# Kernel tuning notes

Measured on AMD Instinct MI355X. Metric: run time of the kernel, lower is better.

Reference implementation:

```python
import jax, jax.numpy as jnp
import numpy as np
from jax import lax

B, N, G, K, D = 16, 8192, 512, 32, 128
MLP = [128, 128, 256]
EPS = 1e-5


def setup_inputs() -> dict:
    key = jax.random.key(0)
    ks = jax.random.split(key, 2 + len(MLP))
    inp = {
        "xyz": jax.random.normal(ks[0], (B, N, 3), jnp.float32),
        "points": jax.random.normal(ks[1], (B, N, D), jnp.float32),
    }
    last = D
    for li, oc in enumerate(MLP, 1):
        inp[f"W{li}"] = jax.random.normal(ks[1 + li], (oc, last), jnp.float32) / np.float32(np.sqrt(last))
        inp[f"b{li}"] = jnp.zeros((oc,), jnp.float32)
        inp[f"g{li}"] = jnp.ones((oc,), jnp.float32)
        inp[f"be{li}"] = jnp.zeros((oc,), jnp.float32)
        last = oc
    return inp


def _fps(xyz, num_group):
    # farthest point sampling, deterministic start at index 0 -> idx [B, G]
    b, n, _ = xyz.shape
    init_idx = jnp.zeros((b,), jnp.int32)

    def step(carry, _):
        dists, last_idx = carry                                   # [B,N], [B]
        last = jnp.take_along_axis(xyz, last_idx[:, None, None], axis=1)  # [B,1,3]
        d = jnp.sum((xyz - last) ** 2, axis=-1)                   # [B,N]
        dists = jnp.minimum(dists, d)
        nxt = jnp.argmax(dists, axis=1).astype(jnp.int32)
        return (dists, nxt), nxt

    init = (jnp.full((b, n), 1e10, jnp.float32), init_idx)
    _, rest = lax.scan(step, init, None, length=num_group - 1)    # [G-1, B]
    return jnp.concatenate([init_idx[None, :], rest], axis=0).T   # [B, G]


def _forward(xyz, points, layers):
    b = xyz.shape[0]
    center_idx = _fps(xyz, G)                                       # [B,G]
    center = jnp.take_along_axis(xyz, center_idx[:, :, None], axis=1)  # [B,G,3]
    # KNN: pairwise squared distances center->points, top-k smallest
    d2 = (jnp.sum(center ** 2, -1)[:, :, None]
          + jnp.sum(xyz ** 2, -1)[:, None, :]
          - 2.0 * jnp.einsum("bgc,bnc->bgn", center, xyz))          # [B,G,N]
    _, idx = lax.top_k(-d2, K)                                      # [B,G,K]
    feats = jnp.take_along_axis(points, idx.reshape(b, G * K, 1), axis=1)
    feats = feats.reshape(b, G, K, -1)                              # [B,G,K,D]
    x = feats.transpose(0, 3, 2, 1)                                 # [B,D,K,G]
    for (W, bb, g, be) in layers:
        x = jnp.einsum("oc,bckg->bokg", W, x) + bb[None, :, None, None]
        m = jnp.mean(x, axis=(0, 2, 3), keepdims=True)
        v = jnp.var(x, axis=(0, 2, 3), keepdims=True)               # biased, as torch BN
        x = (x - m) * lax.rsqrt(v + EPS) * g[None, :, None, None] + be[None, :, None, None]
        x = jax.nn.relu(x)
    new_points = jnp.max(x, axis=2).transpose(0, 2, 1)              # [B,G,C_out]
    return center, new_points


def reference(xyz, points, W1, b1, g1, be1, W2, b2, g2, be2, W3, b3, g3, be3):
    layers = [(W1, b1, g1, be1), (W2, b2, g2, be2), (W3, b3, g3, be3)]
    return _forward(xyz, points, layers)
```

## Files before the change

kernel.cpp:

```cpp
#include <hip/hip_runtime.h>
#include <hip/hip_bf16.h>

#define BB 16
#define NN 8192
#define GG 512
#define KK 32
#define DD 128

typedef __attribute__((ext_vector_type(8))) short bf16x8;
typedef __attribute__((ext_vector_type(4))) float f32x4;
typedef __attribute__((ext_vector_type(2))) float f32x2;
typedef __attribute__((ext_vector_type(2))) unsigned int u32x2;
typedef __attribute__((ext_vector_type(4))) unsigned int u32x4;
typedef __attribute__((ext_vector_type(2))) unsigned long long u64x2;

__device__ __forceinline__ unsigned short f2bf(float f){
  unsigned int u = __builtin_bit_cast(unsigned int, f);
  unsigned int r = (u + 0x7FFFu + ((u >> 16) & 1u)) >> 16;
  return (unsigned short)r;
}
__device__ __forceinline__ float bf2f(unsigned short h){
  unsigned int u = ((unsigned int)h) << 16;
  return __builtin_bit_cast(float, u);
}

__device__ __forceinline__ float wave_max_f32(float v){
  int x = __builtin_bit_cast(int, v);
#define STEPMAX(C) { int y = __builtin_amdgcn_update_dpp(x, x, C, 0xF, 0xF, false); \
  float f = fmaxf(__builtin_bit_cast(float,x), __builtin_bit_cast(float,y)); x = __builtin_bit_cast(int,f); }
  STEPMAX(0x111) STEPMAX(0x112) STEPMAX(0x114) STEPMAX(0x118) STEPMAX(0x142) STEPMAX(0x143)
#undef STEPMAX
  return __builtin_bit_cast(float, __builtin_amdgcn_readlane(x, 63));
}
__device__ __forceinline__ float wave_min_f32(float v){
  int x = __builtin_bit_cast(int, v);
#define STEPMIN(C) { int y = __builtin_amdgcn_update_dpp(x, x, C, 0xF, 0xF, false); \
  float f = fminf(__builtin_bit_cast(float,x), __builtin_bit_cast(float,y)); x = __builtin_bit_cast(int,f); }
  STEPMIN(0x111) STEPMIN(0x112) STEPMIN(0x114) STEPMIN(0x118) STEPMIN(0x142) STEPMIN(0x143)
#undef STEPMIN
  return __builtin_bit_cast(float, __builtin_amdgcn_readlane(x, 63));
}
__device__ __forceinline__ int wave_min_i32(int v){
  int x = v;
#define STEPMNI(C) { int y = __builtin_amdgcn_update_dpp(x, x, C, 0xF, 0xF, false); \
  x = (y < x) ? y : x; }
  STEPMNI(0x111) STEPMNI(0x112) STEPMNI(0x114) STEPMNI(0x118) STEPMNI(0x142) STEPMNI(0x143)
#undef STEPMNI
  return __builtin_amdgcn_readlane(x, 63);
}

__device__ __forceinline__ void knn_group(int bg, int t128,
    const float* __restrict__ xs, const float* __restrict__ ys,
    const float* __restrict__ zs, const float* __restrict__ pps,
    const float* __restrict__ center, int* __restrict__ kidx,
    unsigned long long (*wlist)[KK], int* outidx)
{
#pragma clang fp contract(off)
  int lane = t128 & 63, w = t128 >> 6;
  int b = bg >> 9;
  const float cx = center[(size_t)bg*3+0];
  const float cy = center[(size_t)bg*3+1];
  const float cz = center[(size_t)bg*3+2];
  const float ccv = (cx*cx + cy*cy) + cz*cz;
  const float* xb = xs  + (size_t)b*NN;
  const float* yb = ys  + (size_t)b*NN;
  const float* zb = zs  + (size_t)b*NN;
  const float* pb = pps + (size_t)b*NN;

  f32x2 d2v[32];
  float gmin[8]; int gidx[8];
#pragma unroll
  for (int gi = 0; gi < 8; ++gi){ gmin[gi] = 3.4e38f; gidx[gi] = 0x7FFFFFFF; }
  int nb = w*128 + 2*lane;
  f32x2 cxv = (f32x2){cx, cx}, cyv = (f32x2){cy, cy}, czv = (f32x2){cz, cz};
  f32x2 ccvv = (f32x2){ccv, ccv};
#pragma unroll
  for (int q = 0; q < 32; ++q){
    int n0 = q*256 + nb;
    f32x2 x = *(const f32x2*)(xb + n0);
    f32x2 y = *(const f32x2*)(yb + n0);
    f32x2 z = *(const f32x2*)(zb + n0);
    f32x2 pp = *(const f32x2*)(pb + n0);
    f32x2 dot = (cxv*x + cyv*y) + czv*z;
    f32x2 d = (ccvv + pp) - 2.0f*dot;
    d2v[q] = d;
    int gi = q >> 2;
    if (d.x < gmin[gi]){ gmin[gi] = d.x; gidx[gi] = n0; }
    if (d.y < gmin[gi]){ gmin[gi] = d.y; gidx[gi] = n0 + 1; }
  }
  float bv = gmin[0]; int bi = gidx[0];
#pragma unroll
  for (int gi = 1; gi < 8; ++gi)
    if (gmin[gi] < bv){ bv = gmin[gi]; bi = gidx[gi]; }

  unsigned long long mykey = ~0ULL;
  for (int k = 0; k < KK; ++k){
    float wmin = wave_min_f32(bv);
    unsigned long long mask = __ballot(bv == wmin);
    int n_win;
    if (__popcll(mask) == 1){
      n_win = __builtin_amdgcn_readlane(bi, (int)__builtin_ctzll(mask));
    } else {
      int cand = (bv == wmin) ? bi : 0x7FFFFFFF;
      n_win = wave_min_i32(cand);
    }
    if (lane == k){
      unsigned int fm = __builtin_bit_cast(unsigned int, wmin);
      unsigned int mapd = fm ^ (unsigned int)(((int)fm >> 31) | 0x80000000);
      mykey = ((unsigned long long)mapd << 32) | (unsigned int)n_win;
    }
    if (bi == n_win){
#define RESCAN2(GI) { \
      float nm = 3.4e38f; int ni = 0x7FFFFFFF; \
      _Pragma("unroll") \
      for (int j = 0; j < 4; ++j){ \
        int q = GI*4 + j; \
        int n0 = q*256 + nb; \
        f32x2 v = d2v[q]; \
        if (n0 == n_win) v.x = 3.4e38f; \
        if (n0 + 1 == n_win) v.y = 3.4e38f; \
        d2v[q] = v; \
        if (v.x < nm){ nm = v.x; ni = n0; } \
        if (v.y < nm){ nm = v.y; ni = n0 + 1; } } \
      gmin[GI] = nm; gidx[GI] = ni; }
      switch (n_win >> 10){
        case 0: RESCAN2(0); break;
        case 1: RESCAN2(1); break;
        case 2: RESCAN2(2); break;
        case 3: RESCAN2(3); break;
        case 4: RESCAN2(4); break;
        case 5: RESCAN2(5); break;
        case 6: RESCAN2(6); break;
        default: RESCAN2(7); break;
      }
#undef RESCAN2
      bv = gmin[0]; bi = gidx[0];
#pragma unroll
      for (int gi = 1; gi < 8; ++gi)
        if (gmin[gi] < bv){ bv = gmin[gi]; bi = gidx[gi]; }
    }
  }

  if (lane < KK) wlist[w][lane] = mykey;
  __syncthreads();
  if (lane < KK){
    unsigned long long K = mykey;
    const unsigned long long* other = wlist[1 - w];
    int cnt = 0;
#pragma unroll
    for (int j = 0; j < KK; ++j) cnt += (other[j] < K) ? 1 : 0;
    int rank = lane + cnt;
    if (rank < KK) outidx[rank] = (int)(unsigned int)K;
  }
  __syncthreads();
  if (t128 < KK) kidx[(size_t)bg*KK + t128] = outidx[t128];
}

__global__ __launch_bounds__(1024)
void fps_a_kernel(const float* __restrict__ xyz, const float* __restrict__ points,
                  const float* __restrict__ W1, const float* __restrict__ W2,
                  const float* __restrict__ W3,
                  float* __restrict__ center_out, float* __restrict__ ddws,
                  float* __restrict__ xs, float* __restrict__ ys,
                  float* __restrict__ zs, float* __restrict__ pps,
                  unsigned short* __restrict__ Wbf,
                  unsigned short* __restrict__ pointsbf)
{
#pragma clang fp contract(off)
  __shared__ unsigned long long slot[3][2] __attribute__((aligned(16)));
  __shared__ float tbl[NN][4] __attribute__((aligned(16)));
  __shared__ float outbuf[GG][4] __attribute__((aligned(16)));
  int t = threadIdx.x;
  if (blockIdx.x >= BB){
    int pb = blockIdx.x - BB;
    size_t i = ((size_t)pb*1024 + t)*8;
    f32x4 u0 = *(const f32x4*)(points + i);
    f32x4 u1 = *(const f32x4*)(points + i + 4);
    unsigned int w0 = f2bf(u0[0]) | ((unsigned int)f2bf(u0[1]) << 16);
    unsigned int w1 = f2bf(u0[2]) | ((unsigned int)f2bf(u0[3]) << 16);
    unsigned int w2 = f2bf(u1[0]) | ((unsigned int)f2bf(u1[1]) << 16);
    unsigned int w3 = f2bf(u1[2]) | ((unsigned int)f2bf(u1[3]) << 16);
    u32x4 pv = {w0, w1, w2, w3};
    *(u32x4*)(pointsbf + i) = pv;
    if (pb < 128){
      int n = pb*1024 + t;
      float x = xyz[(size_t)n*3 + 0];
      float y = xyz[(size_t)n*3 + 1];
      float z = xyz[(size_t)n*3 + 2];
      xs[n] = x; ys[n] = y; zs[n] = z;
      pps[n] = (x*x + y*y) + z*z;
    }
    if (pb < 64){
      int n = pb*1024 + t;
      float v;
      if (n < 16384)      v = W1[n];
      else if (n < 32768) v = W2[n - 16384];
      else                v = W3[n - 32768];
      Wbf[n] = f2bf(v);
    }
    return;
  }
  int b = blockIdx.x;
  int lane = t & 63, wid = t >> 6;
  const float* base = xyz + (size_t)b * NN * 3;
  f32x2 px[4], py[4], pz[4], dd[4];
#pragma unroll
  for (int i = 0; i < 4; ++i){
    int n0 = i*2048 + t, n1 = n0 + 1024;
    float x0 = base[n0*3+0], y0 = base[n0*3+1], z0 = base[n0*3+2];
    float x1 = base[n1*3+0], y1 = base[n1*3+1], z1 = base[n1*3+2];
    px[i] = (f32x2){x0, x1}; py[i] = (f32x2){y0, y1}; pz[i] = (f32x2){z0, z1};
    dd[i] = (f32x2){1e10f, 1e10f};
    f32x4 c0 = {x0, y0, z0, 0.f}, c1 = {x1, y1, z1, 0.f};
    *(f32x4*)&tbl[n0][0] = c0;
    *(f32x4*)&tbl[n1][0] = c1;
  }
  float lx = base[0], ly = base[1], lz = base[2];
  if (t < 6) slot[t >> 1][t & 1] = 0;
  if (t == 0){
    f32x4 ob = {lx, ly, lz, 0.f};
    *(f32x4*)&outbuf[0][0] = ob;
  }
  __syncthreads();
  for (int g = 1; g < 256; ++g){
    f32x2 lxv = (f32x2){lx, lx}, lyv = (f32x2){ly, ly}, lzv = (f32x2){lz, lz};
    f32x2 vm = (f32x2){-1.f, -1.f};
#pragma unroll
    for (int i = 0; i < 4; ++i){
      f32x2 dx = px[i] - lxv, dy = py[i] - lyv, dz = pz[i] - lzv;
      f32x2 s = (dx*dx + dy*dy) + dz*dz;
      f32x2 nd = __builtin_elementwise_min(dd[i], s);
      dd[i] = nd;
      vm = __builtin_elementwise_max(vm, nd);
    }
    float m = fmaxf(vm.x, vm.y);
    int mi = 0x7FFFFFFF;
#pragma unroll
    for (int i = 3; i >= 0; --i){
      int n0 = i*2048 + t;
      if (dd[i].y == m) mi = n0 + 1024;
      if (dd[i].x == m) mi = n0;
    }
    float wmax = wave_max_f32(m);
    bool cnd = (m == wmax);
    unsigned long long mask = __ballot(cnd);
    int n_wave;
    if (__popcll(mask) == 1){
      n_wave = __builtin_amdgcn_readlane(mi, (int)__builtin_ctzll(mask));
    } else {
      int cand = cnd ? mi : 0x7FFFFFFF;
      n_wave = wave_min_i32(cand);
    }
    unsigned long long key =
        ((unsigned long long)__builtin_bit_cast(unsigned int, wmax) << 32)
      | (unsigned int)(~n_wave);
    int p = g - (g/3)*3;
    if (lane == 0) atomicMax(&slot[p][wid & 1], key);
    __syncthreads();
    u64x2 sA = *(const u64x2*)&slot[p][0];
    unsigned long long M = sA.x > sA.y ? sA.x : sA.y;
    int n_win = (int)~((unsigned int)M);
    f32x4 cw = *(const f32x4*)&tbl[n_win][0];
    lx = cw[0]; ly = cw[1]; lz = cw[2];
    if (t == 0) *(f32x4*)&outbuf[g][0] = cw;
    if (t < 2){
      int z = p + 2; if (z >= 3) z -= 3;
      slot[z][t] = 0;
    }
  }
  __syncthreads();
  if (t < 256){
    center_out[((size_t)b*GG + t)*3 + 0] = outbuf[t][0];
    center_out[((size_t)b*GG + t)*3 + 1] = outbuf[t][1];
    center_out[((size_t)b*GG + t)*3 + 2] = outbuf[t][2];
  }
  f32x4 s0 = {dd[0].x, dd[0].y, dd[1].x, dd[1].y};
  f32x4 s1 = {dd[2].x, dd[2].y, dd[3].x, dd[3].y};
  float* dp = ddws + ((size_t)b*1024 + t)*8;
  *(f32x4*)dp       = s0;
  *(f32x4*)(dp + 4) = s1;
}

__global__ __launch_bounds__(1024)
void fps_b_kernel(const float* __restrict__ xyz, float* __restrict__ center_out,
                  const float* __restrict__ ddws,
                  const float* __restrict__ xs, const float* __restrict__ ys,
                  const float* __restrict__ zs, const float* __restrict__ pps,
                  int* __restrict__ kidx)
{
#pragma clang fp contract(off)
  __shared__ unsigned long long slot[3][2] __attribute__((aligned(16)));
  __shared__ float tbl[NN][4] __attribute__((aligned(16)));
  __shared__ float outbuf[GG][4] __attribute__((aligned(16)));
  __shared__ unsigned long long kwl[8][2][KK] __attribute__((aligned(16)));
  __shared__ int kout[8][KK];
  int t = threadIdx.x;
  if (blockIdx.x >= BB){
    int pb = blockIdx.x - BB;
    int sub = t >> 7, t128 = t & 127;
    int idx = pb*8 + sub;
    int b = idx >> 8, g = idx & 255;
    knn_group(b*GG + g, t128, xs, ys, zs, pps, center_out, kidx,
              kwl[sub], kout[sub]);
    return;
  }
  int b = blockIdx.x;
  int lane = t & 63, wid = t >> 6;
  const float* base = xyz + (size_t)b * NN * 3;
  f32x2 px[4], py[4], pz[4], dd[4];
  const float* dp = ddws + ((size_t)b*1024 + t)*8;
  f32x4 s0 = *(const f32x4*)dp;
  f32x4 s1 = *(const f32x4*)(dp + 4);
  dd[0] = (f32x2){s0[0], s0[1]};
  dd[1] = (f32x2){s0[2], s0[3]};
  dd[2] = (f32x2){s1[0], s1[1]};
  dd[3] = (f32x2){s1[2], s1[3]};
#pragma unroll
  for (int i = 0; i < 4; ++i){
    int n0 = i*2048 + t, n1 = n0 + 1024;
    float x0 = base[n0*3+0], y0 = base[n0*3+1], z0 = base[n0*3+2];
    float x1 = base[n1*3+0], y1 = base[n1*3+1], z1 = base[n1*3+2];
    px[i] = (f32x2){x0, x1}; py[i] = (f32x2){y0, y1}; pz[i] = (f32x2){z0, z1};
    f32x4 c0 = {x0, y0, z0, 0.f}, c1 = {x1, y1, z1, 0.f};
    *(f32x4*)&tbl[n0][0] = c0;
    *(f32x4*)&tbl[n1][0] = c1;
  }
  float lx = center_out[((size_t)b*GG + 255)*3 + 0];
  float ly = center_out[((size_t)b*GG + 255)*3 + 1];
  float lz = center_out[((size_t)b*GG + 255)*3 + 2];
  if (t < 6) slot[t >> 1][t & 1] = 0;
  __syncthreads();
  for (int g = 256; g < GG; ++g){
    f32x2 lxv = (f32x2){lx, lx}, lyv = (f32x2){ly, ly}, lzv = (f32x2){lz, lz};
    f32x2 vm = (f32x2){-1.f, -1.f};
#pragma unroll
    for (int i = 0; i < 4; ++i){
      f32x2 dx = px[i] - lxv, dy = py[i] - lyv, dz = pz[i] - lzv;
      f32x2 s = (dx*dx + dy*dy) + dz*dz;
      f32x2 nd = __builtin_elementwise_min(dd[i], s);
      dd[i] = nd;
      vm = __builtin_elementwise_max(vm, nd);
    }
    float m = fmaxf(vm.x, vm.y);
    int mi = 0x7FFFFFFF;
#pragma unroll
    for (int i = 3; i >= 0; --i){
      int n0 = i*2048 + t;
      if (dd[i].y == m) mi = n0 + 1024;
      if (dd[i].x == m) mi = n0;
    }
    float wmax = wave_max_f32(m);
    bool cnd = (m == wmax);
    unsigned long long mask = __ballot(cnd);
    int n_wave;
    if (__popcll(mask) == 1){
      n_wave = __builtin_amdgcn_readlane(mi, (int)__builtin_ctzll(mask));
    } else {
      int cand = cnd ? mi : 0x7FFFFFFF;
      n_wave = wave_min_i32(cand);
    }
    unsigned long long key =
        ((unsigned long long)__builtin_bit_cast(unsigned int, wmax) << 32)
      | (unsigned int)(~n_wave);
    int p = g - (g/3)*3;
    if (lane == 0) atomicMax(&slot[p][wid & 1], key);
    __syncthreads();
    u64x2 sA = *(const u64x2*)&slot[p][0];
    unsigned long long M = sA.x > sA.y ? sA.x : sA.y;
    int n_win = (int)~((unsigned int)M);
    f32x4 cw = *(const f32x4*)&tbl[n_win][0];
    lx = cw[0]; ly = cw[1]; lz = cw[2];
    if (t == 0) *(f32x4*)&outbuf[g][0] = cw;
    if (t < 2){
      int z = p + 2; if (z >= 3) z -= 3;
      slot[z][t] = 0;
    }
  }
  __syncthreads();
  if (t < 256){
    int g = 256 + t;
    center_out[((size_t)b*GG + g)*3 + 0] = outbuf[g][0];
    center_out[((size_t)b*GG + g)*3 + 1] = outbuf[g][1];
    center_out[((size_t)b*GG + g)*3 + 2] = outbuf[g][2];
  }
}

__global__ __launch_bounds__(128)
void knn_kernel(const float* __restrict__ xs, const float* __restrict__ ys,
                const float* __restrict__ zs, const float* __restrict__ pps,
                const float* __restrict__ center, int* __restrict__ kidx)
{
  __shared__ unsigned long long kwl[2][KK] __attribute__((aligned(16)));
  __shared__ int kout[KK];
  int idx = blockIdx.x;
  int b = idx >> 8, g = 256 + (idx & 255);
  knn_group(b*GG + g, threadIdx.x, xs, ys, zs, pps, center, kidx, kwl, kout);
}

__global__ __launch_bounds__(256)
void apply_kernel(unsigned short* __restrict__ Y, const float* __restrict__ psum,
                  const float* __restrict__ g, const float* __restrict__ be)
{
  __shared__ float ssc[128], ssh[128];
  int t = threadIdx.x;
  if (t < 128){
    float s = 0.f, q = 0.f;
#pragma unroll
    for (int sl = 0; sl < 64; ++sl){
      s += psum[sl*128 + t];
      q += psum[64*128 + sl*128 + t];
    }
    const float inv = 1.f / 262144.f;
    float mean = s * inv;
    float var  = q * inv - mean*mean;
    float sc = g[t] * rsqrtf(var + 1e-5f);
    ssc[t] = sc;
    ssh[t] = be[t] - mean*sc;
  }
  __syncthreads();
  int f0 = blockIdx.x * 256 + t;
  int c0 = (f0 & 15) * 8;
  f32x4 sA = *(const f32x4*)&ssc[c0];
  f32x4 sB = *(const f32x4*)&ssc[c0 + 4];
  f32x4 hA = *(const f32x4*)&ssh[c0];
  f32x4 hB = *(const f32x4*)&ssh[c0 + 4];
  float sc[8] = {sA[0],sA[1],sA[2],sA[3],sB[0],sB[1],sB[2],sB[3]};
  float sh[8] = {hA[0],hA[1],hA[2],hA[3],hB[0],hB[1],hB[2],hB[3]};
#pragma unroll
  for (int it = 0; it < 8; ++it){
    size_t f = (size_t)f0 + (size_t)it * 524288;
    u32x4 v = *(const u32x4*)(Y + f*8);
    unsigned int wo[4];
#pragma unroll
    for (int p = 0; p < 2; ++p){
#pragma unroll
      for (int w2 = 0; w2 < 2; ++w2){
        int wi = 2*p + w2;
        float x0 = bf2f((unsigned short)(v[wi] & 0xFFFFu));
        float x1 = bf2f((unsigned short)(v[wi] >> 16));
        int cb = 4*p + 2*w2;
        x0 = fmaxf(fmaf(x0, sc[cb],     sh[cb]),     0.f);
        x1 = fmaxf(fmaf(x1, sc[cb + 1], sh[cb + 1]), 0.f);
        wo[wi] = f2bf(x0) | ((unsigned int)f2bf(x1) << 16);
      }
    }
    u32x4 pv = {wo[0], wo[1], wo[2], wo[3]};
    *(u32x4*)(Y + f*8) = pv;
  }
}

template<int OC, int MODE, bool STATS, bool STORE, bool POOL>
__global__ __launch_bounds__(256)
void gemm_kernel(const unsigned short* __restrict__ Wbf, const float* __restrict__ bias,
                 const unsigned short* __restrict__ pointsbf, const int* __restrict__ kidx,
                 const unsigned short* __restrict__ Xin,
                 unsigned short* __restrict__ Yout, float* __restrict__ psum,
                 float* __restrict__ rawmax, float* __restrict__ rawmin)
{
  constexpr int MF = OC / 64;
  __shared__ unsigned short smem[64 * OC];
  int t = threadIdx.x;
  int l = t & 63, w = t >> 6;
  int l15 = l & 15, lh = l >> 4;
  int sbid = (blockIdx.x & 7) * 512 + (blockIdx.x >> 3);
  int jbase = sbid * 64;
  int obase = w * (OC / 4);

  bf16x8 a[MF][4];
#pragma unroll
  for (int m = 0; m < MF; ++m)
#pragma unroll
    for (int kf = 0; kf < 4; ++kf){
      int row = obase + m*16 + l15;
      int c8  = kf*32 + lh*8;
      a[m][kf] = *(const bf16x8*)(Wbf + (size_t)row*128 + c8);
    }

#pragma unroll
  for (int q = 0; q < 4; ++q){
    int ci = q*256 + t;
    int j = ci >> 4, cc = ci & 15;
    unsigned short* dst = &smem[j*128 + ((cc ^ (j & 15)) * 8)];
    if constexpr (MODE == 0){
      int jg = jbase + j;
      int bb = jg >> 14;
      int row = kidx[jg];
      const unsigned short* src = pointsbf + ((size_t)bb*NN + row)*DD + cc*8;
      *(u32x4*)dst = *(const u32x4*)src;
    } else {
      const unsigned short* src = Xin + ((size_t)(jbase + j))*128 + cc*8;
      *(u32x4*)dst = *(const u32x4*)src;
    }
  }
  __syncthreads();

  f32x4 acc[MF][4];
#pragma unroll
  for (int m = 0; m < MF; ++m)
#pragma unroll
    for (int n = 0; n < 4; ++n)
      acc[m][n] = (f32x4){0.f, 0.f, 0.f, 0.f};

#pragma unroll
  for (int n = 0; n < 4; ++n){
    bf16x8 bfr[4];
    int j = n*16 + l15;
#pragma unroll
    for (int kf = 0; kf < 4; ++kf){
      int ch = kf*4 + lh;
      bfr[kf] = *(const bf16x8*)&smem[j*128 + ((ch ^ (j & 15)) * 8)];
    }
#pragma unroll
    for (int m = 0; m < MF; ++m)
#pragma unroll
      for (int kf = 0; kf < 4; ++kf)
        acc[m][n] = __builtin_amdgcn_mfma_f32_16x16x32_bf16(a[m][kf], bfr[kf], acc[m][n], 0, 0, 0);
  }

#pragma unroll
  for (int m = 0; m < MF; ++m){
    int o0 = obase + m*16 + lh*4;
    f32x4 bv = *(const f32x4*)(bias + o0);
#pragma unroll
    for (int n = 0; n < 4; ++n) acc[m][n] += bv;
  }

  if constexpr (STATS){
    int slot = blockIdx.x & 63;
#pragma unroll
    for (int m = 0; m < MF; ++m){
#pragma unroll
      for (int r = 0; r < 4; ++r){
        float s = 0.f, q2 = 0.f;
#pragma unroll
        for (int n = 0; n < 4; ++n){ float v = acc[m][n][r]; s += v; q2 += v*v; }
        s  += __shfl_xor(s, 1);  s  += __shfl_xor(s, 2);  s  += __shfl_xor(s, 4);  s  += __shfl_xor(s, 8);
        q2 += __shfl_xor(q2, 1); q2 += __shfl_xor(q2, 2); q2 += __shfl_xor(q2, 4); q2 += __shfl_xor(q2, 8);
        if (l15 == 0){
          int o = obase + m*16 + lh*4 + r;
          atomicAdd(psum + slot*OC + o, s);
          atomicAdd(psum + 64*OC + slot*OC + o, q2);
        }
      }
    }
  }

  if constexpr (POOL){
#pragma unroll
    for (int m = 0; m < MF; ++m){
      int o0 = obase + m*16 + lh*4;
      f32x4 gmx0, gmx1, gmn0, gmn1;
#pragma unroll
      for (int r = 0; r < 4; ++r){
        float v0 = acc[m][0][r], v1 = acc[m][1][r];
        float v2 = acc[m][2][r], v3 = acc[m][3][r];
        float ax0 = fmaxf(v0, v1), ax1 = fmaxf(v2, v3);
        float an0 = fminf(v0, v1), an1 = fminf(v2, v3);
#pragma unroll
        for (int mk = 1; mk < 16; mk <<= 1){
          ax0 = fmaxf(ax0, __shfl_xor(ax0, mk));
          ax1 = fmaxf(ax1, __shfl_xor(ax1, mk));
          an0 = fminf(an0, __shfl_xor(an0, mk));
          an1 = fminf(an1, __shfl_xor(an1, mk));
        }
        gmx0[r] = ax0; gmx1[r] = ax1; gmn0[r] = an0; gmn1[r] = an1;
      }
      if (l15 == 0){
        int gg = jbase >> 5;
        *(f32x4*)(rawmax + (size_t)gg*256 + o0)       = gmx0;
        *(f32x4*)(rawmax + (size_t)(gg + 1)*256 + o0) = gmx1;
        *(f32x4*)(rawmin + (size_t)gg*256 + o0)       = gmn0;
        *(f32x4*)(rawmin + (size_t)(gg + 1)*256 + o0) = gmn1;
      }
    }
  }

  if constexpr (STORE){
    __syncthreads();
#pragma unroll
    for (int m = 0; m < MF; ++m){
      int o0 = obase + m*16 + lh*4;
      int co = o0 >> 2;
#pragma unroll
      for (int n = 0; n < 4; ++n){
        int j = n*16 + l15;
        unsigned int w0 = f2bf(acc[m][n][0]) | ((unsigned int)f2bf(acc[m][n][1]) << 16);
        unsigned int w1 = f2bf(acc[m][n][2]) | ((unsigned int)f2bf(acc[m][n][3]) << 16);
        u32x2 pv = {w0, w1};
        *(u32x2*)&smem[j*OC + ((co ^ ((j & 15) << 1)) * 4)] = pv;
      }
    }
    __syncthreads();
    constexpr int CPR = OC / 4;
    constexpr int CPT = (64 * CPR) / 256;
#pragma unroll
    for (int q = 0; q < CPT; ++q){
      int ci = q*256 + t;
      int j = ci / CPR, co = ci % CPR;
      u32x2 v = *(const u32x2*)&smem[j*OC + ((co ^ ((j & 15) << 1)) * 4)];
      *(u32x2*)(Yout + (size_t)(jbase + j)*OC + co*4) = v;
    }
  }
}

__global__ __launch_bounds__(256)
void finish3_kernel(const float* __restrict__ psumC, const float* __restrict__ g3,
                    const float* __restrict__ be3, const float* __restrict__ rawmax,
                    const float* __restrict__ rawmin, float* __restrict__ opool)
{
  __shared__ float ssc[256], ssh[256];
  int t = threadIdx.x;
  {
    float s = 0.f, q = 0.f;
#pragma unroll
    for (int sl = 0; sl < 64; ++sl){
      s += psumC[sl*256 + t];
      q += psumC[64*256 + sl*256 + t];
    }
    const float inv = 1.f / 262144.f;
    float mean = s * inv;
    float var  = q * inv - mean*mean;
    float sc = g3[t] * rsqrtf(var + 1e-5f);
    ssc[t] = sc;
    ssh[t] = be3[t] - mean*sc;
  }
  __syncthreads();
  float sc = ssc[t], sh = ssh[t];
  int gg0 = blockIdx.x * 16;
#pragma unroll
  for (int i = 0; i < 16; ++i){
    int gg = gg0 + i;
    float rv = (sc >= 0.f) ? rawmax[(size_t)gg*256 + t] : rawmin[(size_t)gg*256 + t];
    opool[(size_t)gg*256 + t] = fmaxf(fmaf(rv, sc, sh), 0.f);
  }
}

extern "C" void kernel_launch(void* const* d_in, const int* in_sizes, int n_in,
                              void* d_out, int out_size, void* d_ws, size_t ws_size,
                              hipStream_t stream)
{
  const float* xyz    = (const float*)d_in[0];
  const float* points = (const float*)d_in[1];
  const float* W1  = (const float*)d_in[2];
  const float* b1  = (const float*)d_in[3];
  const float* g1  = (const float*)d_in[4];
  const float* be1 = (const float*)d_in[5];
  const float* W2  = (const float*)d_in[6];
  const float* b2  = (const float*)d_in[7];
  const float* g2  = (const float*)d_in[8];
  const float* be2 = (const float*)d_in[9];
  const float* W3  = (const float*)d_in[10];
  const float* b3  = (const float*)d_in[11];
  const float* g3  = (const float*)d_in[12];
  const float* be3 = (const float*)d_in[13];

  float* out    = (float*)d_out;
  float* center = out;
  float* opool  = out + (size_t)BB*GG*3;

  char* ws = (char*)d_ws;
  size_t off = 0;
  auto alloc = [&](size_t bytes) -> void* {
    void* p = ws + off;
    off += (bytes + 255) & ~(size_t)255;
    return p;
  };
  unsigned short* Y1   = (unsigned short*)alloc((size_t)262144*128*2);
  unsigned short* Y2   = (unsigned short*)alloc((size_t)262144*128*2);
  int*   kidx = (int*)  alloc((size_t)262144*4);
  unsigned short* Wbf = (unsigned short*)alloc((size_t)65536*2);
  float* rawmax = (float*)alloc((size_t)8192*256*4);
  float* rawmin = (float*)alloc((size_t)8192*256*4);
  float* psumA = (float*)alloc((size_t)2*64*128*4);
  float* psumB = (float*)alloc((size_t)2*64*128*4);
  float* psumC = (float*)alloc((size_t)2*64*256*4);
  float* xsb  = (float*)alloc((size_t)131072*4);
  float* ysb  = (float*)alloc((size_t)131072*4);
  float* zsb  = (float*)alloc((size_t)131072*4);
  float* ppsb = (float*)alloc((size_t)131072*4);
  float* ddws = (float*)alloc((size_t)16*1024*8*4);
  unsigned short* pointsbf = Y2;

  hipMemsetAsync(psumA, 0, (size_t)(2*64*128 + 2*64*128 + 2*64*256)*4 + 1024, stream);

  fps_a_kernel<<<BB + 2048, 1024, 0, stream>>>(
      xyz, points, W1, W2, W3, center, ddws, xsb, ysb, zsb, ppsb, Wbf, pointsbf);
  fps_b_kernel<<<BB + 512, 1024, 0, stream>>>(
      xyz, center, ddws, xsb, ysb, zsb, ppsb, kidx);
  knn_kernel<<<4096, 128, 0, stream>>>(xsb, ysb, zsb, ppsb, center, kidx);

  gemm_kernel<128, 0, true, true, false><<<4096, 256, 0, stream>>>(
      Wbf, b1, pointsbf, kidx, nullptr, Y1, psumA, nullptr, nullptr);
  apply_kernel<<<2048, 256, 0, stream>>>(Y1, psumA, g1, be1);

  gemm_kernel<128, 1, true, true, false><<<4096, 256, 0, stream>>>(
      Wbf + 16384, b2, nullptr, nullptr, Y1, Y2, psumB, nullptr, nullptr);
  apply_kernel<<<2048, 256, 0, stream>>>(Y2, psumB, g2, be2);

  gemm_kernel<256, 1, true, false, true><<<4096, 256, 0, stream>>>(
      Wbf + 32768, b3, nullptr, nullptr, Y2, nullptr, psumC, rawmax, rawmin);

  finish3_kernel<<<512, 256, 0, stream>>>(psumC, g3, be3, rawmax, rawmin, opool);
}
```

Before: 764.9 us.

## Fuse BN-apply into next GEMM load and overlap KNN with first GEMM

Removes the standalone apply kernels by folding the BatchNorm scale/shift and ReLU into the input-staging step of the following GEMM, with each block recomputing the scale/shift from the partial sums. Also merges the second-half KNN with the first GEMM over first-half groups (whose KNN indices were already computed earlier) into one launch, then runs the remaining GEMM1 tiles in a separate launch. This saves two read-modify-write passes over the activations and some launch gaps. The cost is redundant per-block stat reduction and more complex block-index remapping.

```diff
diff --git a/kernel.cpp b/kernel.cpp
--- a/kernel.cpp
+++ b/kernel.cpp
@@ -385,86 +385,39 @@
   }
 }
 
-__global__ __launch_bounds__(128)
-void knn_kernel(const float* __restrict__ xs, const float* __restrict__ ys,
-                const float* __restrict__ zs, const float* __restrict__ pps,
-                const float* __restrict__ center, int* __restrict__ kidx)
-{
-  __shared__ unsigned long long kwl[2][KK] __attribute__((aligned(16)));
-  __shared__ int kout[KK];
-  int idx = blockIdx.x;
-  int b = idx >> 8, g = 256 + (idx & 255);
-  knn_group(b*GG + g, threadIdx.x, xs, ys, zs, pps, center, kidx, kwl, kout);
-}
-
-__global__ __launch_bounds__(256)
-void apply_kernel(unsigned short* __restrict__ Y, const float* __restrict__ psum,
-                  const float* __restrict__ g, const float* __restrict__ be)
-{
-  __shared__ float ssc[128], ssh[128];
-  int t = threadIdx.x;
-  if (t < 128){
-    float s = 0.f, q = 0.f;
-#pragma unroll
-    for (int sl = 0; sl < 64; ++sl){
-      s += psum[sl*128 + t];
-      q += psum[64*128 + sl*128 + t];
-    }
-    const float inv = 1.f / 262144.f;
-    float mean = s * inv;
-    float var  = q * inv - mean*mean;
-    float sc = g[t] * rsqrtf(var + 1e-5f);
-    ssc[t] = sc;
-    ssh[t] = be[t] - mean*sc;
-  }
-  __syncthreads();
-  int f0 = blockIdx.x * 256 + t;
-  int c0 = (f0 & 15) * 8;
-  f32x4 sA = *(const f32x4*)&ssc[c0];
-  f32x4 sB = *(const f32x4*)&ssc[c0 + 4];
-  f32x4 hA = *(const f32x4*)&ssh[c0];
-  f32x4 hB = *(const f32x4*)&ssh[c0 + 4];
-  float sc[8] = {sA[0],sA[1],sA[2],sA[3],sB[0],sB[1],sB[2],sB[3]};
-  float sh[8] = {hA[0],hA[1],hA[2],hA[3],hB[0],hB[1],hB[2],hB[3]};
-#pragma unroll
-  for (int it = 0; it < 8; ++it){
-    size_t f = (size_t)f0 + (size_t)it * 524288;
-    u32x4 v = *(const u32x4*)(Y + f*8);
-    unsigned int wo[4];
-#pragma unroll
-    for (int p = 0; p < 2; ++p){
-#pragma unroll
-      for (int w2 = 0; w2 < 2; ++w2){
-        int wi = 2*p + w2;
-        float x0 = bf2f((unsigned short)(v[wi] & 0xFFFFu));
-        float x1 = bf2f((unsigned short)(v[wi] >> 16));
-        int cb = 4*p + 2*w2;
-        x0 = fmaxf(fmaf(x0, sc[cb],     sh[cb]),     0.f);
-        x1 = fmaxf(fmaf(x1, sc[cb + 1], sh[cb + 1]), 0.f);
-        wo[wi] = f2bf(x0) | ((unsigned int)f2bf(x1) << 16);
-      }
-    }
-    u32x4 pv = {wo[0], wo[1], wo[2], wo[3]};
-    *(u32x4*)(Y + f*8) = pv;
-  }
-}
-
 template<int OC, int MODE, bool STATS, bool STORE, bool POOL>
-__global__ __launch_bounds__(256)
-void gemm_kernel(const unsigned short* __restrict__ Wbf, const float* __restrict__ bias,
-                 const unsigned short* __restrict__ pointsbf, const int* __restrict__ kidx,
-                 const unsigned short* __restrict__ Xin,
-                 unsigned short* __restrict__ Yout, float* __restrict__ psum,
-                 float* __restrict__ rawmax, float* __restrict__ rawmin)
+__device__ __forceinline__ void gemm_body(int sbid, int t, int slot,
+    const unsigned short* __restrict__ Wbf, const float* __restrict__ bias,
+    const unsigned short* __restrict__ pointsbf, const int* __restrict__ kidx,
+    const unsigned short* __restrict__ Xin,
+    const float* __restrict__ psum_in, const float* __restrict__ gin,
+    const float* __restrict__ bein,
+    unsigned short* __restrict__ Yout, float* __restrict__ psum,
+    float* __restrict__ rawmax, float* __restrict__ rawmin,
+    unsigned short* smem, float* ssc, float* ssh)
 {
   constexpr int MF = OC / 64;
-  __shared__ unsigned short smem[64 * OC];
-  int t = threadIdx.x;
   int l = t & 63, w = t >> 6;
   int l15 = l & 15, lh = l >> 4;
-  int sbid = (blockIdx.x & 7) * 512 + (blockIdx.x >> 3);
   int jbase = sbid * 64;
   int obase = w * (OC / 4);
+
+  if constexpr (MODE == 1){
+    if (t < 128){
+      float s = 0.f, q = 0.f;
+#pragma unroll
+      for (int sl = 0; sl < 64; ++sl){
+        s += psum_in[sl*128 + t];
+        q += psum_in[64*128 + sl*128 + t];
+      }
+      const float inv = 1.f / 262144.f;
+      float mean = s * inv;
+      float var  = q * inv - mean*mean;
+      float sc = gin[t] * rsqrtf(var + 1e-5f);
+      ssc[t] = sc;
+      ssh[t] = bein[t] - mean*sc;
+    }
+  }
 
   bf16x8 a[MF][4];
 #pragma unroll
@@ -475,6 +428,8 @@
       int c8  = kf*32 + lh*8;
       a[m][kf] = *(const bf16x8*)(Wbf + (size_t)row*128 + c8);
     }
+
+  if constexpr (MODE == 1) __syncthreads();
 
 #pragma unroll
   for (int q = 0; q < 4; ++q){
@@ -489,7 +444,19 @@
       *(u32x4*)dst = *(const u32x4*)src;
     } else {
       const unsigned short* src = Xin + ((size_t)(jbase + j))*128 + cc*8;
-      *(u32x4*)dst = *(const u32x4*)src;
+      u32x4 v = *(const u32x4*)src;
+      int c0 = cc * 8;
+      unsigned int wo[4];
+#pragma unroll
+      for (int p = 0; p < 4; ++p){
+        float x0 = bf2f((unsigned short)(v[p] & 0xFFFFu));
+        float x1 = bf2f((unsigned short)(v[p] >> 16));
+        x0 = fmaxf(fmaf(x0, ssc[c0 + 2*p],     ssh[c0 + 2*p]),     0.f);
+        x1 = fmaxf(fmaf(x1, ssc[c0 + 2*p + 1], ssh[c0 + 2*p + 1]), 0.f);
+        wo[p] = f2bf(x0) | ((unsigned int)f2bf(x1) << 16);
+      }
+      u32x4 pv = {wo[0], wo[1], wo[2], wo[3]};
+      *(u32x4*)dst = pv;
     }
   }
   __syncthreads();
@@ -526,7 +493,6 @@
   }
 
   if constexpr (STATS){
-    int slot = blockIdx.x & 63;
 #pragma unroll
     for (int m = 0; m < MF; ++m){
 #pragma unroll
@@ -601,6 +567,62 @@
       *(u32x2*)(Yout + (size_t)(jbase + j)*OC + co*4) = v;
     }
   }
+}
+
+__global__ __launch_bounds__(256)
+void knn_gemm1_kernel(const float* __restrict__ xs, const float* __restrict__ ys,
+                      const float* __restrict__ zs, const float* __restrict__ pps,
+                      const float* __restrict__ center, int* __restrict__ kidx,
+                      const unsigned short* __restrict__ Wbf,
+                      const float* __restrict__ b1,
+                      const unsigned short* __restrict__ pointsbf,
+                      unsigned short* __restrict__ Y1, float* __restrict__ psumA)
+{
+  __shared__ unsigned short smem[64 * 128];
+  __shared__ unsigned long long kwl[2][2][KK] __attribute__((aligned(16)));
+  __shared__ int kout[2][KK];
+  int bid = blockIdx.x, t = threadIdx.x;
+  if (bid < 2048){
+    int swz = (bid & 7) * 256 + (bid >> 3);
+    int sub = t >> 7, t128 = t & 127;
+    int idx = swz*2 + sub;
+    int b = idx >> 8, g = 256 + (idx & 255);
+    knn_group(b*GG + g, t128, xs, ys, zs, pps, center, kidx,
+              kwl[sub], kout[sub]);
+    return;
+  }
+  int h = bid - 2048;
+  int hs = (h & 7) * 256 + (h >> 3);
+  int sbid = (hs >> 7) * 256 + (hs & 127);
+  gemm_body<128, 0, true, true, false>(sbid, t, bid & 63,
+      Wbf, b1, pointsbf, kidx, nullptr, nullptr, nullptr, nullptr,
+      Y1, psumA, nullptr, nullptr, smem, nullptr, nullptr);
+}
+
+template<int OC, int MODE, bool STATS, bool STORE, bool POOL>
+__global__ __launch_bounds__(256)
+void gemm_kernel(int gridmode,
+                 const unsigned short* __restrict__ Wbf, const float* __restrict__ bias,
+                 const unsigned short* __restrict__ pointsbf, const int* __restrict__ kidx,
+                 const unsigned short* __restrict__ Xin,
+                 const float* __restrict__ psum_in, const float* __restrict__ gin,
+                 const float* __restrict__ bein,
+                 unsigned short* __restrict__ Yout, float* __restrict__ psum,
+                 float* __restrict__ rawmax, float* __restrict__ rawmin)
+{
+  __shared__ unsigned short smem[64 * OC];
+  __shared__ float ssc[128], ssh[128];
+  int bid = blockIdx.x, t = threadIdx.x;
+  int sbid;
+  if (gridmode == 0){
+    sbid = (bid & 7) * 512 + (bid >> 3);
+  } else {
+    int hs = (bid & 7) * 256 + (bid >> 3);
+    sbid = (hs >> 7) * 256 + 128 + (hs & 127);
+  }
+  gemm_body<OC, MODE, STATS, STORE, POOL>(sbid, t, bid & 63,
+      Wbf, bias, pointsbf, kidx, Xin, psum_in, gin, bein,
+      Yout, psum, rawmax, rawmin, smem, ssc, ssh);
 }
 
 __global__ __launch_bounds__(256)
@@ -687,18 +709,21 @@
       xyz, points, W1, W2, W3, center, ddws, xsb, ysb, zsb, ppsb, Wbf, pointsbf);
   fps_b_kernel<<<BB + 512, 1024, 0, stream>>>(
       xyz, center, ddws, xsb, ysb, zsb, ppsb, kidx);
-  knn_kernel<<<4096, 128, 0, stream>>>(xsb, ysb, zsb, ppsb, center, kidx);
-
-  gemm_kernel<128, 0, true, true, false><<<4096, 256, 0, stream>>>(
-      Wbf, b1, pointsbf, kidx, nullptr, Y1, psumA, nullptr, nullptr);
-  apply_kernel<<<2048, 256, 0, stream>>>(Y1, psumA, g1, be1);
+
+  knn_gemm1_kernel<<<4096, 256, 0, stream>>>(
+      xsb, ysb, zsb, ppsb, center, kidx, Wbf, b1, pointsbf, Y1, psumA);
+
+  gemm_kernel<128, 0, true, true, false><<<2048, 256, 0, stream>>>(
+      2, Wbf, b1, pointsbf, kidx, nullptr, nullptr, nullptr, nullptr,
+      Y1, psumA, nullptr, nullptr);
 
   gemm_kernel<128, 1, true, true, false><<<4096, 256, 0, stream>>>(
-      Wbf + 16384, b2, nullptr, nullptr, Y1, Y2, psumB, nullptr, nullptr);
-  apply_kernel<<<2048, 256, 0, stream>>>(Y2, psumB, g2, be2);
+      0, Wbf + 16384, b2, nullptr, nullptr, Y1, psumA, g1, be1,
+      Y2, psumB, nullptr, nullptr);
 
   gemm_kernel<256, 1, true, false, true><<<4096, 256, 0, stream>>>(
-      Wbf + 32768, b3, nullptr, nullptr, Y2, nullptr, psumC, rawmax, rawmin);
+      0, Wbf + 32768, b3, nullptr, nullptr, Y2, psumB, g2, be2,
+      nullptr, psumC, rawmax, rawmin);
 
   finish3_kernel<<<512, 256, 0, stream>>>(psumC, g3, be3, rawmax, rawmin, opool);
 }
```

New measurement: 779.3 us. No clear change (+1.9%).
